# Kernel optimization log

Measured on AMD Instinct MI355X. Metric: run time of the kernel, lower is better.

## Reference

```python
import jax, jax.numpy as jnp
import numpy as np
from jax import lax

N, C, H, W = 16, 1, 512, 512
MAX_ITERS = H + W  # upper bound on flood-fill propagation distance


def _dilate4(r):
    # 3x3 cross (4-connectivity) grayscale dilation, r: (N,H,W)
    rp = jnp.pad(r, ((0, 0), (1, 1), (1, 1)))
    up = rp[:, :-2, 1:-1]
    dn = rp[:, 2:, 1:-1]
    lf = rp[:, 1:-1, :-2]
    rt = rp[:, 1:-1, 2:]
    return jnp.maximum(jnp.maximum(jnp.maximum(up, dn), jnp.maximum(lf, rt)), r)


def _reconstruct_dilation(marker, mask):
    # skimage.morphology.reconstruction(seed, mask, method='dilation'):
    # iterate rec = min(dilate(rec), mask) until convergence.
    def cond(state):
        _, changed, i = state
        return jnp.logical_and(changed, i < MAX_ITERS)

    def body(state):
        r, _, i = state
        nr = jnp.minimum(_dilate4(r), mask)
        return nr, jnp.any(nr != r), i + 1

    rec, _, _ = lax.while_loop(cond, body, (marker, jnp.array(True), jnp.array(0)))
    return rec


def _adaptive_binarize(prob, marker_factor, mask_factor):
    # prob: (N,1,H,W); mirrors torch .detach() -> threshold -> reconstruction
    img = lax.stop_gradient(prob[:, 0])  # (N,H,W)
    nzm = img > 0
    cnt = jnp.sum(nzm, axis=(1, 2))                      # (N,)
    safe = jnp.maximum(cnt, 1).astype(img.dtype)
    mean = jnp.sum(jnp.where(nzm, img, 0.0), axis=(1, 2)) / safe
    var = jnp.sum(jnp.where(nzm, (img - mean[:, None, None]) ** 2, 0.0), axis=(1, 2)) / safe
    std = jnp.sqrt(var)

    def threshold(factor):
        T = (mean + factor * std)[:, None, None]
        b = img > T
        empty = jnp.sum(b, axis=(1, 2)) == 0
        T2 = (mean + (factor / 2.0) * std)[:, None, None]
        b2 = img > T2
        return jnp.where(empty[:, None, None], b2, b)

    marker = threshold(marker_factor).astype(jnp.float32)
    maskb = threshold(mask_factor).astype(jnp.float32)
    rec = _reconstruct_dilation(marker, maskb)
    out = (rec > 0.5).astype(jnp.float32)
    out = jnp.where((cnt == 0)[:, None, None], 0.0, out)  # no nonzero pixels -> zeros
    return out[:, None]  # (N,1,H,W)


def setup_inputs() -> dict:
    key = jax.random.key(0)
    k1, k2 = jax.random.split(key)
    thick_logit = jax.random.normal(k1, (N, C, H, W), dtype=jnp.float32)
    thin_logit = jax.random.normal(k2, (N, C, H, W), dtype=jnp.float32)
    return {"thick_logit": thick_logit, "thin_logit": thin_logit}


def reference(thick_logit, thin_logit):
    thick_prob = jax.nn.sigmoid(thick_logit)
    thin_prob = jax.nn.sigmoid(thin_logit)
    thick_bin = _adaptive_binarize(thick_prob, 2.0, 0.5)
    thin_bin = _adaptive_binarize(thin_prob, 4.0, 0.5)
    fused_bin = jnp.clip(thick_bin + thin_bin, 0.0, 1.0)
    return thick_logit, thin_logit, fused_bin
```

## Files before the change

### kernel.cpp

```cpp
#include <hip/hip_runtime.h>
#include <cstdint>
#include <cstddef>

#define HW 512
#define NPIX (HW * HW)
#define NIMG 16
#define NII 32
#define CHUNKS 64
#define CHUNK_PIX 4096
#define IN_ELEMS (NIMG * NPIX)
#define WPI 4096

typedef unsigned long long u64;

#define WS_PARTA 0u
#define WS_CUT   49152u
#define WS_ZM    49664u
#define WS_PARTC 49920u
#define WS_MP    98304u
#define WS_MF    (WS_MP + 1048576u)
#define WS_KP    (WS_MF + 1048576u)
#define WS_KF    (WS_KP + 1048576u)
#define WS_ROUT  (WS_KF + 1048576u)

__device__ __forceinline__ float sigmoid_f32(float x) {
    return (float)(1.0 / (1.0 + exp(-(double)x)));
}

__global__ void k1_stats(const float* __restrict__ A, const float* __restrict__ B,
                         double* __restrict__ partA) {
    int b = blockIdx.x;
    int ii = b >> 6, chunk = b & 63;
    const float* src = ((ii >> 4) == 0 ? A : B) + (size_t)(ii & 15) * NPIX
                     + (size_t)chunk * CHUNK_PIX;
    double s = 0.0, sq = 0.0, c = 0.0;
#pragma unroll
    for (int p = 0; p < 4; ++p) {
        float4 v = *(const float4*)(src + p * 1024 + threadIdx.x * 4);
        float xs[4] = {v.x, v.y, v.z, v.w};
#pragma unroll
        for (int q = 0; q < 4; ++q) {
            float img = sigmoid_f32(xs[q]);
            if (img > 0.0f) { double d = (double)img; s += d; sq += d * d; c += 1.0; }
        }
    }
    __shared__ double sm[256], sv[256], sc[256];
    sm[threadIdx.x] = s; sv[threadIdx.x] = sq; sc[threadIdx.x] = c;
    __syncthreads();
    for (int off = 128; off > 0; off >>= 1) {
        if (threadIdx.x < off) {
            sm[threadIdx.x] += sm[threadIdx.x + off];
            sv[threadIdx.x] += sv[threadIdx.x + off];
            sc[threadIdx.x] += sc[threadIdx.x + off];
        }
        __syncthreads();
    }
    if (threadIdx.x == 0) {
        double* p = partA + (size_t)(ii * 64 + chunk) * 3;
        p[0] = sm[0]; p[1] = sv[0]; p[2] = sc[0];
    }
}

__device__ __forceinline__ float key_to_f32(unsigned k) {
    unsigned b = (k & 0x80000000u) ? (k ^ 0x80000000u) : ~k;
    return __uint_as_float(b);
}
__device__ float find_cut(double T) {
    if (!(1.0 > T)) return __uint_as_float(0x7F800000u);
    unsigned lo = 0x007FFFFFu;
    unsigned hi = 0xFF800000u;
    while (lo < hi) {
        unsigned mid = lo + ((hi - lo) >> 1);
        float x = key_to_f32(mid);
        float s32 = sigmoid_f32(x);
        if ((double)s32 > T) hi = mid; else lo = mid + 1;
    }
    return key_to_f32(lo);
}

__global__ void kS_cut(const double* __restrict__ partA,
                       float* __restrict__ cut, u64* __restrict__ zm) {
    int ii = blockIdx.x, t = threadIdx.x;
    const double* p = partA + (size_t)(ii * 64 + t) * 3;
    double s = p[0], sq = p[1], c = p[2];
    for (int off = 32; off > 0; off >>= 1) {
        s  += __shfl_down(s,  (unsigned)off, 64);
        sq += __shfl_down(sq, (unsigned)off, 64);
        c  += __shfl_down(c,  (unsigned)off, 64);
    }
    s = __shfl(s, 0, 64); sq = __shfl(sq, 0, 64); c = __shfl(c, 0, 64);
    double mean = 0.0, sd = 0.0;
    if (c > 0.0) {
        mean = s / c;
        double var = sq / c - mean * mean;
        if (var < 0.0) var = 0.0;
        sd = sqrt(var);
    }
    double fac = (ii < 16) ? 2.0 : 4.0;
    if (t < 4) {
        double T = (t == 0) ? mean + fac * sd
                 : (t == 1) ? mean + 0.5 * fac * sd
                 : (t == 2) ? mean + 0.5 * sd
                 :            mean + 0.25 * sd;
        cut[ii * 4 + t] = find_cut(T);
    }
    if (t == 0) zm[ii] = (c > 0.0) ? ~0ull : 0ull;
}

__global__ void k2_bits(const float* __restrict__ A, const float* __restrict__ B,
                        const float* __restrict__ cut,
                        u64* __restrict__ mp, u64* __restrict__ mf,
                        u64* __restrict__ kp, u64* __restrict__ kf,
                        long long* __restrict__ partC, float* __restrict__ out) {
    int b = blockIdx.x, ii = b >> 6, chunk = b & 63;
    int j = ii >> 4, n = ii & 15;
    const float* src = (j == 0 ? A : B) + (size_t)n * NPIX;
    float* dst = out + (size_t)j * IN_ELEMS + (size_t)n * NPIX;
    float cM = cut[ii * 4 + 0], cMf = cut[ii * 4 + 1];
    float cK = cut[ii * 4 + 2], cKf = cut[ii * 4 + 3];

    int t = threadIdx.x, lane = t & 63, w = t >> 6;
    long long aM = 0, aK = 0;
#pragma unroll 4
    for (int i = 0; i < 16; ++i) {
        int e = chunk * CHUNK_PIX + i * 256 + t;
        float x = src[e];
        dst[e] = x;
        u64 bM  = __ballot(x >= cM);
        u64 bMf = __ballot(x >= cMf);
        u64 bK  = __ballot(x >= cK);
        u64 bKf = __ballot(x >= cKf);
        if (lane == 0) {
            size_t g = (size_t)ii * WPI + (size_t)chunk * 64 + i * 4 + w;
            mp[g] = bM; mf[g] = bMf; kp[g] = bK; kf[g] = bKf;
            aM += (long long)__popcll(bM);
            aK += (long long)__popcll(bK);
        }
    }
    __shared__ long long sM[4], sK[4];
    if (lane == 0) { sM[w] = aM; sK[w] = aK; }
    __syncthreads();
    if (t == 0) {
        long long* p = partC + (size_t)(ii * 64 + chunk) * 2;
        p[0] = sM[0] + sM[1] + sM[2] + sM[3];
        p[1] = sK[0] + sK[1] + sK[2] + sK[3];
    }
}

__device__ __forceinline__ void hfill8(u64* x, const u64* k) {
    u64 c = 0;
#pragma unroll
    for (int w = 0; w < 8; ++w) {
        u64 a = k[w], g = x[w];
        u64 t1 = a + g;  u64 c1 = (u64)(t1 < a);
        u64 t2 = t1 + c; u64 c2 = (u64)(t2 < t1);
        c = c1 | c2;
        x[w] = (~t2 | g) & a;
    }
    c = 0;
#pragma unroll
    for (int w = 7; w >= 0; --w) {
        u64 a = __brevll(k[w]), g = __brevll(x[w]);
        u64 t1 = a + g;  u64 c1 = (u64)(t1 < a);
        u64 t2 = t1 + c; u64 c2 = (u64)(t2 < t1);
        c = c1 | c2;
        x[w] = __brevll((~t2 | g) & a);
    }
}

__global__ __launch_bounds__(512) void k3_flood(
        const u64* __restrict__ mp, const u64* __restrict__ mf,
        const u64* __restrict__ kp, const u64* __restrict__ kf,
        const long long* __restrict__ partC, u64* __restrict__ rout) {
    int ii = blockIdx.x, t = threadIdx.x;
    __shared__ u64 R[8 * HW];
    __shared__ int ssel[2];

    if (t < 64) {
        long long a = partC[(size_t)(ii * 64 + t) * 2];
        long long b = partC[(size_t)(ii * 64 + t) * 2 + 1];
        for (int off = 32; off > 0; off >>= 1) {
            a += __shfl_down(a, (unsigned)off, 64);
            b += __shfl_down(b, (unsigned)off, 64);
        }
        if (t == 0) { ssel[0] = (a == 0); ssel[1] = (b == 0); }
    }
    __syncthreads();
    const u64* M = (ssel[0] ? mf : mp) + (size_t)ii * WPI;
    const u64* K = (ssel[1] ? kf : kp) + (size_t)ii * WPI;

    u64 r[8], k[8];
#pragma unroll
    for (int w = 0; w < 8; ++w) {
        k[w] = K[(size_t)t * 8 + w];
        r[w] = M[(size_t)t * 8 + w] & k[w];
    }
    hfill8(r, k);
#pragma unroll
    for (int w = 0; w < 8; ++w) R[w * HW + t] = r[w];
    __syncthreads();

    for (int it = 0; it < 1024; ++it) {
        u64 up[8], dn[8];
#pragma unroll
        for (int w = 0; w < 8; ++w) {
            up[w] = (t > 0)      ? R[w * HW + (t - 1)] : 0ull;
            dn[w] = (t < HW - 1) ? R[w * HW + (t + 1)] : 0ull;
        }
        __syncthreads();
        u64 diff = 0;
#pragma unroll
        for (int w = 0; w < 8; ++w) {
            u64 g = (up[w] | dn[w]) & k[w] & ~r[w];
            r[w] |= g; diff |= g;
        }
        if (diff) {
            hfill8(r, k);
#pragma unroll
            for (int w = 0; w < 8; ++w) R[w * HW + t] = r[w];
        }
        if (!__syncthreads_or(diff != 0ull ? 1 : 0)) break;
    }

#pragma unroll
    for (int w = 0; w < 8; ++w)
        rout[(size_t)ii * WPI + (size_t)w * HW + t] = r[w];
}

__global__ void k4_fuse(const u64* __restrict__ rout,
                        const u64* __restrict__ zm,
                        float* __restrict__ out) {
    size_t gid = (size_t)blockIdx.x * blockDim.x + threadIdx.x;
    size_t p = gid * 4;
    int n = (int)(p >> 18);
    int e = (int)(p & (NPIX - 1));
    size_t gw = (size_t)(((e >> 6) & 7) * HW + (e >> 9));
    u64 w = (rout[(size_t)n * WPI + gw] & zm[n])
          | (rout[(size_t)(16 + n) * WPI + gw] & zm[16 + n]);
    int sh = e & 63;
    float4 v;
    v.x = ((w >> sh) & 1ull)       ? 1.0f : 0.0f;
    v.y = ((w >> (sh + 1)) & 1ull) ? 1.0f : 0.0f;
    v.z = ((w >> (sh + 2)) & 1ull) ? 1.0f : 0.0f;
    v.w = ((w >> (sh + 3)) & 1ull) ? 1.0f : 0.0f;
    *(float4*)(out + 2 * (size_t)IN_ELEMS + p) = v;
}

extern "C" void kernel_launch(void* const* d_in, const int* in_sizes, int n_in,
                              void* d_out, int out_size, void* d_ws, size_t ws_size,
                              hipStream_t stream) {
    const float* thick = (const float*)d_in[0];
    const float* thin  = (const float*)d_in[1];
    float* out = (float*)d_out;
    char* ws = (char*)d_ws;

    double*    partA = (double*)(ws + WS_PARTA);
    float*     cut   = (float*)(ws + WS_CUT);
    u64*       zm    = (u64*)(ws + WS_ZM);
    long long* partC = (long long*)(ws + WS_PARTC);
    u64*       mp    = (u64*)(ws + WS_MP);
    u64*       mf    = (u64*)(ws + WS_MF);
    u64*       kp    = (u64*)(ws + WS_KP);
    u64*       kf    = (u64*)(ws + WS_KF);
    u64*       rout  = (u64*)(ws + WS_ROUT);

    k1_stats<<<NII * CHUNKS, 256, 0, stream>>>(thick, thin, partA);
    kS_cut<<<NII, 64, 0, stream>>>(partA, cut, zm);
    k2_bits<<<NII * CHUNKS, 256, 0, stream>>>(thick, thin, cut, mp, mf, kp, kf, partC, out);
    k3_flood<<<NII, 512, 0, stream>>>(mp, mf, kp, kf, partC, rout);
    k4_fuse<<<4096, 256, 0, stream>>>(rout, zm, out);
}
```

Baseline: 151.8 us.

## Pick threshold fallback via max reduction, move input copy into stats pass

The stats kernel now also copies the inputs to the output, tracks a per-image max logit, and uses a hand-rolled double-precision exp polynomial in place of the library exp. kS_cut uses that max to decide whether the primary threshold is empty and picks one cut per marker and one per mask. As a result k2_bits writes two bitmaps instead of four, and k3_flood no longer reduces popcounts to choose a bitmap. The aim is less global bitmap traffic, cheaper sigmoid evaluation and a shorter setup in the flood kernel. The risk is that the fast exp rounds slightly differently from the library exp, which could move the mean and std near the thresholds.

```diff
diff --git a/kernel.cpp b/kernel.cpp
--- a/kernel.cpp
+++ b/kernel.cpp
@@ -14,50 +14,78 @@
 typedef unsigned long long u64;
 
 #define WS_PARTA 0u
-#define WS_CUT   49152u
-#define WS_ZM    49664u
-#define WS_PARTC 49920u
-#define WS_MP    98304u
-#define WS_MF    (WS_MP + 1048576u)
-#define WS_KP    (WS_MF + 1048576u)
-#define WS_KF    (WS_KP + 1048576u)
-#define WS_ROUT  (WS_KF + 1048576u)
+#define WS_CUT   65536u
+#define WS_ZM    65792u
+#define WS_MSEL  98304u
+#define WS_KSEL  (WS_MSEL + 1048576u)
+#define WS_ROUT  (WS_KSEL + 1048576u)
 
 __device__ __forceinline__ float sigmoid_f32(float x) {
     return (float)(1.0 / (1.0 + exp(-(double)x)));
 }
 
-__global__ void k1_stats(const float* __restrict__ A, const float* __restrict__ B,
-                         double* __restrict__ partA) {
+__device__ __forceinline__ float sigmoid_fast(float xf) {
+    double x = (double)xf;
+    double y = x * -1.4426950408889634074;
+    if (y > 1000.0)  return 0.0f;
+    if (y < -1000.0) return 1.0f;
+    double n = __builtin_rint(y);
+    double t = (y - n) * 0.69314718055994530942;
+    double p = 2.5052108385441718775e-8;
+    p = __builtin_fma(p, t, 2.7557319223985890653e-7);
+    p = __builtin_fma(p, t, 2.7557319223985892511e-6);
+    p = __builtin_fma(p, t, 2.4801587301587301566e-5);
+    p = __builtin_fma(p, t, 1.9841269841269841253e-4);
+    p = __builtin_fma(p, t, 1.3888888888888889419e-3);
+    p = __builtin_fma(p, t, 8.3333333333333332177e-3);
+    p = __builtin_fma(p, t, 4.1666666666666664354e-2);
+    p = __builtin_fma(p, t, 1.6666666666666665741e-1);
+    p = __builtin_fma(p, t, 5.0e-1);
+    p = __builtin_fma(p, t, 1.0);
+    p = __builtin_fma(p, t, 1.0);
+    long long bits = ((long long)n + 1023ll) << 52;
+    double e = p * __longlong_as_double(bits);
+    return (float)(1.0 / (1.0 + e));
+}
+
+__global__ void k1_copy_stats(const float* __restrict__ A, const float* __restrict__ B,
+                              float* __restrict__ out, double* __restrict__ partA) {
     int b = blockIdx.x;
     int ii = b >> 6, chunk = b & 63;
-    const float* src = ((ii >> 4) == 0 ? A : B) + (size_t)(ii & 15) * NPIX
-                     + (size_t)chunk * CHUNK_PIX;
-    double s = 0.0, sq = 0.0, c = 0.0;
+    int j = ii >> 4, n = ii & 15;
+    const float* src = (j == 0 ? A : B) + (size_t)n * NPIX + (size_t)chunk * CHUNK_PIX;
+    float* dst = out + (size_t)j * IN_ELEMS + (size_t)n * NPIX + (size_t)chunk * CHUNK_PIX;
+
+    double s = 0.0, sq = 0.0, cc = 0.0;
+    float mx = -__builtin_inff();
 #pragma unroll
     for (int p = 0; p < 4; ++p) {
         float4 v = *(const float4*)(src + p * 1024 + threadIdx.x * 4);
+        *(float4*)(dst + p * 1024 + threadIdx.x * 4) = v;
         float xs[4] = {v.x, v.y, v.z, v.w};
 #pragma unroll
         for (int q = 0; q < 4; ++q) {
-            float img = sigmoid_f32(xs[q]);
-            if (img > 0.0f) { double d = (double)img; s += d; sq += d * d; c += 1.0; }
+            float img = sigmoid_fast(xs[q]);
+            mx = fmaxf(mx, xs[q]);
+            if (img > 0.0f) { double d = (double)img; s += d; sq += d * d; cc += 1.0; }
         }
     }
     __shared__ double sm[256], sv[256], sc[256];
-    sm[threadIdx.x] = s; sv[threadIdx.x] = sq; sc[threadIdx.x] = c;
+    __shared__ float smx[256];
+    sm[threadIdx.x] = s; sv[threadIdx.x] = sq; sc[threadIdx.x] = cc; smx[threadIdx.x] = mx;
     __syncthreads();
     for (int off = 128; off > 0; off >>= 1) {
         if (threadIdx.x < off) {
             sm[threadIdx.x] += sm[threadIdx.x + off];
             sv[threadIdx.x] += sv[threadIdx.x + off];
             sc[threadIdx.x] += sc[threadIdx.x + off];
+            smx[threadIdx.x] = fmaxf(smx[threadIdx.x], smx[threadIdx.x + off]);
         }
         __syncthreads();
     }
     if (threadIdx.x == 0) {
-        double* p = partA + (size_t)(ii * 64 + chunk) * 3;
-        p[0] = sm[0]; p[1] = sv[0]; p[2] = sc[0];
+        double* p = partA + (size_t)(ii * 64 + chunk) * 4;
+        p[0] = sm[0]; p[1] = sv[0]; p[2] = sc[0]; p[3] = (double)smx[0];
     }
 }
 
@@ -79,16 +107,18 @@
 }
 
 __global__ void kS_cut(const double* __restrict__ partA,
-                       float* __restrict__ cut, u64* __restrict__ zm) {
+                       float* __restrict__ cut2, u64* __restrict__ zm) {
     int ii = blockIdx.x, t = threadIdx.x;
-    const double* p = partA + (size_t)(ii * 64 + t) * 3;
-    double s = p[0], sq = p[1], c = p[2];
+    const double* p = partA + (size_t)(ii * 64 + t) * 4;
+    double s = p[0], sq = p[1], c = p[2], mx = p[3];
     for (int off = 32; off > 0; off >>= 1) {
         s  += __shfl_down(s,  (unsigned)off, 64);
         sq += __shfl_down(sq, (unsigned)off, 64);
         c  += __shfl_down(c,  (unsigned)off, 64);
-    }
-    s = __shfl(s, 0, 64); sq = __shfl(sq, 0, 64); c = __shfl(c, 0, 64);
+        mx  = fmax(mx, __shfl_down(mx, (unsigned)off, 64));
+    }
+    s = __shfl(s, 0, 64); sq = __shfl(sq, 0, 64);
+    c = __shfl(c, 0, 64); mx = __shfl(mx, 0, 64);
     double mean = 0.0, sd = 0.0;
     if (c > 0.0) {
         mean = s / c;
@@ -97,53 +127,41 @@
         sd = sqrt(var);
     }
     double fac = (ii < 16) ? 2.0 : 4.0;
+    __shared__ float cs[4];
     if (t < 4) {
         double T = (t == 0) ? mean + fac * sd
                  : (t == 1) ? mean + 0.5 * fac * sd
                  : (t == 2) ? mean + 0.5 * sd
                  :            mean + 0.25 * sd;
-        cut[ii * 4 + t] = find_cut(T);
-    }
-    if (t == 0) zm[ii] = (c > 0.0) ? ~0ull : 0ull;
+        cs[t] = find_cut(T);
+    }
+    __syncthreads();
+    if (t == 0) {
+        float mxf = (float)mx;
+        cut2[ii * 2 + 0] = (mxf >= cs[0]) ? cs[0] : cs[1];
+        cut2[ii * 2 + 1] = (mxf >= cs[2]) ? cs[2] : cs[3];
+        zm[ii] = (c > 0.0) ? ~0ull : 0ull;
+    }
 }
 
 __global__ void k2_bits(const float* __restrict__ A, const float* __restrict__ B,
-                        const float* __restrict__ cut,
-                        u64* __restrict__ mp, u64* __restrict__ mf,
-                        u64* __restrict__ kp, u64* __restrict__ kf,
-                        long long* __restrict__ partC, float* __restrict__ out) {
+                        const float* __restrict__ cut2,
+                        u64* __restrict__ msel, u64* __restrict__ ksel) {
     int b = blockIdx.x, ii = b >> 6, chunk = b & 63;
     int j = ii >> 4, n = ii & 15;
     const float* src = (j == 0 ? A : B) + (size_t)n * NPIX;
-    float* dst = out + (size_t)j * IN_ELEMS + (size_t)n * NPIX;
-    float cM = cut[ii * 4 + 0], cMf = cut[ii * 4 + 1];
-    float cK = cut[ii * 4 + 2], cKf = cut[ii * 4 + 3];
-
+    float cM = cut2[ii * 2 + 0];
+    float cK = cut2[ii * 2 + 1];
     int t = threadIdx.x, lane = t & 63, w = t >> 6;
-    long long aM = 0, aK = 0;
 #pragma unroll 4
     for (int i = 0; i < 16; ++i) {
-        int e = chunk * CHUNK_PIX + i * 256 + t;
-        float x = src[e];
-        dst[e] = x;
-        u64 bM  = __ballot(x >= cM);
-        u64 bMf = __ballot(x >= cMf);
-        u64 bK  = __ballot(x >= cK);
-        u64 bKf = __ballot(x >= cKf);
+        float x = src[chunk * CHUNK_PIX + i * 256 + t];
+        u64 bM = __ballot(x >= cM);
+        u64 bK = __ballot(x >= cK);
         if (lane == 0) {
             size_t g = (size_t)ii * WPI + (size_t)chunk * 64 + i * 4 + w;
-            mp[g] = bM; mf[g] = bMf; kp[g] = bK; kf[g] = bKf;
-            aM += (long long)__popcll(bM);
-            aK += (long long)__popcll(bK);
-        }
-    }
-    __shared__ long long sM[4], sK[4];
-    if (lane == 0) { sM[w] = aM; sK[w] = aK; }
-    __syncthreads();
-    if (t == 0) {
-        long long* p = partC + (size_t)(ii * 64 + chunk) * 2;
-        p[0] = sM[0] + sM[1] + sM[2] + sM[3];
-        p[1] = sK[0] + sK[1] + sK[2] + sK[3];
+            msel[g] = bM; ksel[g] = bK;
+        }
     }
 }
 
@@ -168,26 +186,13 @@
     }
 }
 
-__global__ __launch_bounds__(512) void k3_flood(
-        const u64* __restrict__ mp, const u64* __restrict__ mf,
-        const u64* __restrict__ kp, const u64* __restrict__ kf,
-        const long long* __restrict__ partC, u64* __restrict__ rout) {
+__global__ __launch_bounds__(512) void k3_flood(const u64* __restrict__ msel,
+                                                const u64* __restrict__ ksel,
+                                                u64* __restrict__ rout) {
     int ii = blockIdx.x, t = threadIdx.x;
     __shared__ u64 R[8 * HW];
-    __shared__ int ssel[2];
-
-    if (t < 64) {
-        long long a = partC[(size_t)(ii * 64 + t) * 2];
-        long long b = partC[(size_t)(ii * 64 + t) * 2 + 1];
-        for (int off = 32; off > 0; off >>= 1) {
-            a += __shfl_down(a, (unsigned)off, 64);
-            b += __shfl_down(b, (unsigned)off, 64);
-        }
-        if (t == 0) { ssel[0] = (a == 0); ssel[1] = (b == 0); }
-    }
-    __syncthreads();
-    const u64* M = (ssel[0] ? mf : mp) + (size_t)ii * WPI;
-    const u64* K = (ssel[1] ? kf : kp) + (size_t)ii * WPI;
+    const u64* M = msel + (size_t)ii * WPI;
+    const u64* K = ksel + (size_t)ii * WPI;
 
     u64 r[8], k[8];
 #pragma unroll
@@ -249,24 +254,21 @@
 extern "C" void kernel_launch(void* const* d_in, const int* in_sizes, int n_in,
                               void* d_out, int out_size, void* d_ws, size_t ws_size,
                               hipStream_t stream) {
-    const float* thick = (const float*)d_in[0];
-    const float* thin  = (const float*)d_in[1];
+    const float* A = (const float*)d_in[0];
+    const float* B = (const float*)d_in[1];
     float* out = (float*)d_out;
     char* ws = (char*)d_ws;
 
-    double*    partA = (double*)(ws + WS_PARTA);
-    float*     cut   = (float*)(ws + WS_CUT);
-    u64*       zm    = (u64*)(ws + WS_ZM);
-    long long* partC = (long long*)(ws + WS_PARTC);
-    u64*       mp    = (u64*)(ws + WS_MP);
-    u64*       mf    = (u64*)(ws + WS_MF);
-    u64*       kp    = (u64*)(ws + WS_KP);
-    u64*       kf    = (u64*)(ws + WS_KF);
-    u64*       rout  = (u64*)(ws + WS_ROUT);
-
-    k1_stats<<<NII * CHUNKS, 256, 0, stream>>>(thick, thin, partA);
-    kS_cut<<<NII, 64, 0, stream>>>(partA, cut, zm);
-    k2_bits<<<NII * CHUNKS, 256, 0, stream>>>(thick, thin, cut, mp, mf, kp, kf, partC, out);
-    k3_flood<<<NII, 512, 0, stream>>>(mp, mf, kp, kf, partC, rout);
+    double* partA = (double*)(ws + WS_PARTA);
+    float*  cut2  = (float*)(ws + WS_CUT);
+    u64*    zm    = (u64*)(ws + WS_ZM);
+    u64*    msel  = (u64*)(ws + WS_MSEL);
+    u64*    ksel  = (u64*)(ws + WS_KSEL);
+    u64*    rout  = (u64*)(ws + WS_ROUT);
+
+    k1_copy_stats<<<NII * CHUNKS, 256, 0, stream>>>(A, B, out, partA);
+    kS_cut<<<NII, 64, 0, stream>>>(partA, cut2, zm);
+    k2_bits<<<NII * CHUNKS, 256, 0, stream>>>(A, B, cut2, msel, ksel);
+    k3_flood<<<NII, 512, 0, stream>>>(msel, ksel, rout);
     k4_fuse<<<4096, 256, 0, stream>>>(rout, zm, out);
 }
```

Result: faster. 145.7 us (-4.1%).
